# Kernel optimization log

Measured on AMD Instinct MI355X. Metric: run time of the kernel, lower is better.

## Reference

```python
import jax, jax.numpy as jnp
import numpy as np

B, OBS, ACT_DIM, C, CTX, H = 128, 512, 7, 100, 128, 512
IN = OBS + 1 + CTX  # states + scalar action component + context = 641


def cont2disc(values, n):
    return jnp.clip(jnp.floor((values + 1.0) / 2.0 * n), 0, n - 1)


def setup_inputs() -> dict:
    key = jax.random.key(0)
    ks = jax.random.split(key, 10)
    def w(k, shape):
        return jax.random.normal(k, shape, dtype=jnp.float32) / np.sqrt(shape[-2])
    return {
        "observations": jax.random.normal(ks[0], (B, OBS), dtype=jnp.float32),
        "actions": jax.random.uniform(ks[1], (B, ACT_DIM), dtype=jnp.float32, minval=-1.0, maxval=1.0),
        # one MLP per action dim (weight_sharing=False): layers IN->H->H->CTX
        "W1": w(ks[2], (ACT_DIM, IN, H)),  "b1": jnp.zeros((ACT_DIM, H), jnp.float32),
        "W2": w(ks[3], (ACT_DIM, H, H)),   "b2": jnp.zeros((ACT_DIM, H), jnp.float32),
        "W3": w(ks[4], (ACT_DIM, H, CTX)), "b3": jnp.zeros((ACT_DIM, CTX), jnp.float32),
        # output_proj = MLP((1,)): single dense CTX->1, no activation
        "Wp": w(ks[5], (CTX, 1)), "bp": jnp.zeros((1,), jnp.float32),
        "compute_lse": 1,
    }


def reference(observations, actions, W1, b1, W2, b2, W3, b3, Wp, bp, compute_lse):
    n = observations.shape[0]
    acts = cont2disc(actions, C)  # [B, ACT_DIM], float component indices
    context = jnp.zeros((n, CTX), observations.dtype)
    comp = jnp.arange(C, dtype=observations.dtype)  # candidate components 0..C-1
    q = jnp.zeros((n, ACT_DIM * C), observations.dtype)

    for i in range(1, ACT_DIM):
        def mlp(x, i=i):  # hidden layers relu, final layer linear
            h = jax.nn.relu(x @ W1[i] + b1[i])
            h = jax.nn.relu(h @ W2[i] + b2[i])
            return h @ W3[i] + b3[i]

        # batched over all num_components candidate actions (replaces the per-j loop)
        xin = jnp.concatenate([
            jnp.broadcast_to(observations[:, None, :], (n, C, OBS)),
            jnp.broadcast_to(comp[None, :, None], (n, C, 1)),
            jnp.broadcast_to(context[:, None, :], (n, C, CTX)),
        ], axis=-1)  # [B, C, IN]
        curr_ctx = mlp(xin) + context[:, None, :]        # [B, C, CTX]
        qv = (curr_ctx @ Wp + bp)[..., 0]                # [B, C]
        q = q.at[:, (i - 1) * C : i * C].set(qv)          # which_qval ordering

        # advance context with the actual (discretized) action
        x = jnp.concatenate([observations, acts[:, i:i + 1], context], axis=-1)
        context = mlp(x) + context

    if compute_lse:
        return jax.scipy.special.logsumexp(q, axis=-1)    # [B]
    return context @ Wp + bp                              # [B, 1]
```

## Files before the change

kernel.cpp:

```cpp
#include <hip/hip_runtime.h>
#include <math.h>

#define BATCH 128
#define ACT 7
#define NC 100
#define CTXD 128
#define HID 512
#define QW 600

typedef __attribute__((ext_vector_type(8))) __bf16 bf16x8;
typedef __attribute__((ext_vector_type(4))) float f32x4;
typedef __attribute__((ext_vector_type(4))) unsigned short u16x4;

__device__ __forceinline__ unsigned short f2bf(float f) {
    union { float f; unsigned int u; } v; v.f = f;
    unsigned int u = v.u;
    return (unsigned short)((u + 0x7fffu + ((u >> 16) & 1u)) >> 16);
}
__device__ __forceinline__ unsigned int pack2bf(float a, float b) {
    unsigned int ua = __float_as_uint(a) + 0x8000u;
    unsigned int ub = __float_as_uint(b) + 0x8000u;
    return (ua >> 16) | (ub & 0xffff0000u);
}

__device__ __forceinline__ void async16(const void* g, void* l) {
    __builtin_amdgcn_global_load_lds(
        (const __attribute__((address_space(1))) unsigned int*)(uintptr_t)g,
        (__attribute__((address_space(3))) unsigned int*)(unsigned int)(uintptr_t)l,
        16, 0, 0);
}

__global__ void prep_kernel(const float* __restrict__ obs, const float* __restrict__ W1,
                            const float* __restrict__ W2, const float* __restrict__ W3,
                            const float* __restrict__ Wp,
                            unsigned short* __restrict__ obs_bf, unsigned short* __restrict__ W1Cbf,
                            unsigned short* __restrict__ W2bf, unsigned short* __restrict__ W3bf,
                            unsigned short* __restrict__ W1AT, unsigned short* __restrict__ W2T,
                            float* __restrict__ vq) {
    const int bidx = blockIdx.x, tid = threadIdx.x;
    if (bidx < 2368) {
        const int e = (bidx * 256 + tid) * 4;
        const float* src; unsigned short* dst;
        if (e < 65536)        { src = obs + e; dst = obs_bf + e; }
        else if (e < 458752)  { int f = e - 65536; int i = f >> 16; int rem = f & 65535;
                                src = W1 + (size_t)(i + 1) * 328192 + 513*512 + rem; dst = W1Cbf + f; }
        else if (e < 2031616) { int f = e - 458752; src = W2 + 262144 + f; dst = W2bf + f; }
        else                  { int f = e - 2031616; src = W3 + 65536 + f; dst = W3bf + f; }
        float4 v = *(const float4*)src;
        u16x4 o; o[0] = f2bf(v.x); o[1] = f2bf(v.y); o[2] = f2bf(v.z); o[3] = f2bf(v.w);
        *(u16x4*)dst = o;
    } else if (bidx < 5440) {
        __shared__ float tile[32][33];
        const int idx = bidx - 2368;
        const int z = idx >> 8, rem = idx & 255;
        const int rb = rem & 15, cb = rem >> 4;
        const float* ip; unsigned short* op;
        if (z < 6) { ip = W1 + (size_t)(z + 1) * 328192; op = W1AT + (size_t)z * 262144; }
        else       { int i = z - 6; ip = W2 + (size_t)(i + 1) * 262144; op = W2T + (size_t)i * 262144; }
        const int r0 = rb * 32, c0 = cb * 32;
        const int tx = tid & 31, ty = tid >> 5;
        #pragma unroll
        for (int j = 0; j < 32; j += 8)
            tile[ty + j][tx] = ip[(size_t)(r0 + ty + j) * 512 + c0 + tx];
        __syncthreads();
        #pragma unroll
        for (int j = 0; j < 32; j += 8)
            op[(size_t)(c0 + ty + j) * 512 + r0 + tx] = f2bf(tile[tx][ty + j]);
    } else {
        const int idx = bidx - 5440;
        const int z = idx >> 1, k = (idx & 1) * 256 + tid;
        const float4* row = (const float4*)(W3 + (size_t)(z + 1) * 65536 + (size_t)k * 128);
        const float4* wp4 = (const float4*)Wp;
        float s = 0.f;
        #pragma unroll 8
        for (int n = 0; n < 32; ++n) {
            float4 a = row[n], w = wp4[n];
            s += a.x*w.x + a.y*w.y + a.z*w.z + a.w*w.w;
        }
        vq[z * 512 + k] = s;
    }
}

__launch_bounds__(256)
__global__ void yobs_kernel(const unsigned short* __restrict__ A,
                            const unsigned short* __restrict__ BtAll,
                            const float* __restrict__ b1,
                            float* __restrict__ Yobs) {
    __shared__ unsigned short As[64*32];
    __shared__ unsigned short Bs[128*32];
    const int m0 = blockIdx.x * 64;
    const int n0 = blockIdx.y * 128;
    const int z  = blockIdx.z;
    const unsigned short* Bt = BtAll + (size_t)z * 262144;
    const int tid = threadIdx.x, lane = tid & 63, wave = tid >> 6;
    const int wm = wave >> 1, wn = wave & 1;
    const int srow = tid >> 2, skc = (tid & 3) * 8;
    const unsigned short* gA  = A  + (size_t)(m0 + srow) * HID + skc;
    const unsigned short* gB0 = Bt + (size_t)(n0 + srow) * HID + skc;
    const unsigned short* gB1 = gB0 + 64 * HID;
    f32x4 acc[2][4] = {};
    for (int k0 = 0; k0 < HID; k0 += 32) {
        async16(gA + k0, As + tid*8);
        async16(gB0 + k0, Bs + tid*8);
        async16(gB1 + k0, Bs + 2048 + tid*8);
        __syncthreads();
        const int q8 = (lane >> 4) * 8, l15 = lane & 15;
        bf16x8 af[2], bfr[4];
        #pragma unroll
        for (int mt = 0; mt < 2; ++mt)
            af[mt] = *(const bf16x8*)(As + (wm*32 + mt*16 + l15) * 32 + q8);
        #pragma unroll
        for (int nt = 0; nt < 4; ++nt)
            bfr[nt] = *(const bf16x8*)(Bs + (wn*64 + nt*16 + l15) * 32 + q8);
        #pragma unroll
        for (int mt = 0; mt < 2; ++mt)
            #pragma unroll
            for (int nt = 0; nt < 4; ++nt)
                acc[mt][nt] = __builtin_amdgcn_mfma_f32_16x16x32_bf16(af[mt], bfr[nt], acc[mt][nt], 0, 0, 0);
        __syncthreads();
    }
    const int colL = wn*64 + (lane & 15);
    #pragma unroll
    for (int nt = 0; nt < 4; ++nt) {
        const int col = n0 + colL + nt*16;
        const float bb = b1[(z + 1) * HID + col];
        #pragma unroll
        for (int mt = 0; mt < 2; ++mt)
            #pragma unroll
            for (int r = 0; r < 4; ++r) {
                const int row = m0 + wm*32 + mt*16 + (lane >> 4)*4 + r;
                Yobs[(size_t)z * 65536 + (size_t)row * HID + col] = acc[mt][nt][r] + bb;
            }
    }
}

__launch_bounds__(1024)
__global__ void chain_kernel(const float* __restrict__ Yobs, const float* __restrict__ W1,
                             const unsigned short* __restrict__ W1Cbf,
                             const unsigned short* __restrict__ W2bf,
                             const unsigned short* __restrict__ W3bf,
                             const float* __restrict__ b2, const float* __restrict__ b3,
                             const float* __restrict__ actions,
                             const float* __restrict__ Wp, const float* __restrict__ bp,
                             float* __restrict__ Y0all, float* __restrict__ QOFF) {
    const int b = blockIdx.x, t = threadIdx.x;
    __shared__ float ctx[128], h1[512], h2s[512];
    __shared__ float part[2048];
    const int pair = t & 255, kq = t >> 8;
    const int pair3 = t & 63, kq3 = t >> 6;
    if (t < 128) ctx[t] = 0.f;
    __syncthreads();
    for (int i = 1; i <= 6; ++i) {
        if (t < 128) part[t] = (ctx[t] + b3[i*128 + t]) * Wp[t];
        __syncthreads();
        if (t < 64) {
            float v = part[t] + part[t + 64];
            #pragma unroll
            for (int o = 32; o > 0; o >>= 1) v += __shfl_down(v, o, 64);
            if (t == 0) QOFF[(i-1)*128 + b] = v + bp[0];
        }
        __syncthreads();
        const float a = actions[b*ACT + i];
        float fj = floorf((a + 1.0f) * 50.0f);
        fj = fminf(fmaxf(fj, 0.0f), 99.0f);
        {
            const unsigned int* wp1 = (const unsigned int*)(W1Cbf + (size_t)(i-1)*65536) + pair;
            float acc0 = 0.f, acc1 = 0.f;
            #pragma unroll 8
            for (int k = kq*32; k < kq*32 + 32; ++k) {
                unsigned int u = wp1[k*256];
                float c = ctx[k];
                acc0 = fmaf(c, __uint_as_float(u << 16), acc0);
                acc1 = fmaf(c, __uint_as_float(u & 0xffff0000u), acc1);
            }
            *(float2*)(&part[kq*512 + 2*pair]) = make_float2(acc0, acc1);
        }
        __syncthreads();
        if (t < 256) {
            const int n2 = 2*t;
            float2 p0 = *(const float2*)(&part[n2]);
            float2 p1 = *(const float2*)(&part[512 + n2]);
            float2 p2 = *(const float2*)(&part[1024 + n2]);
            float2 p3 = *(const float2*)(&part[1536 + n2]);
            float2 yo = *(const float2*)(Yobs + (size_t)(i-1)*65536 + b*512 + n2);
            float y0a = yo.x + p0.x + p1.x + p2.x + p3.x;
            float y0b = yo.y + p0.y + p1.y + p2.y + p3.y;
            *(float2*)(Y0all + (size_t)(i-1)*65536 + b*512 + n2) = make_float2(y0a, y0b);
            const float* w1a = W1 + (size_t)i*328192 + 262144;
            float2 wv = *(const float2*)(w1a + n2);
            h1[n2]   = fmaxf(fmaf(fj, wv.x, y0a), 0.f);
            h1[n2+1] = fmaxf(fmaf(fj, wv.y, y0b), 0.f);
        }
        __syncthreads();
        {
            const unsigned int* wp2 = (const unsigned int*)(W2bf + (size_t)(i-1)*262144) + pair;
            float acc0 = 0.f, acc1 = 0.f;
            #pragma unroll 16
            for (int k = kq*128; k < kq*128 + 128; ++k) {
                unsigned int u = wp2[k*256];
                float hv = h1[k];
                acc0 = fmaf(hv, __uint_as_float(u << 16), acc0);
                acc1 = fmaf(hv, __uint_as_float(u & 0xffff0000u), acc1);
            }
            *(float2*)(&part[kq*512 + 2*pair]) = make_float2(acc0, acc1);
        }
        __syncthreads();
        if (t < 256) {
            const int n2 = 2*t;
            float2 p0 = *(const float2*)(&part[n2]);
            float2 p1 = *(const float2*)(&part[512 + n2]);
            float2 p2 = *(const float2*)(&part[1024 + n2]);
            float2 p3 = *(const float2*)(&part[1536 + n2]);
            float2 bb = *(const float2*)(b2 + i*512 + n2);
            h2s[n2]   = fmaxf(p0.x + p1.x + p2.x + p3.x + bb.x, 0.f);
            h2s[n2+1] = fmaxf(p0.y + p1.y + p2.y + p3.y + bb.y, 0.f);
        }
        __syncthreads();
        {
            const unsigned int* wp3 = (const unsigned int*)(W3bf + (size_t)(i-1)*65536) + pair3;
            float acc0 = 0.f, acc1 = 0.f;
            #pragma unroll 8
            for (int k = kq3*32; k < kq3*32 + 32; ++k) {
                unsigned int u = wp3[k*64];
                float hv = h2s[k];
                acc0 = fmaf(hv, __uint_as_float(u << 16), acc0);
                acc1 = fmaf(hv, __uint_as_float(u & 0xffff0000u), acc1);
            }
            *(float2*)(&part[kq3*128 + 2*pair3]) = make_float2(acc0, acc1);
        }
        __syncthreads();
        if (t < 128) {
            float s = 0.f;
            #pragma unroll
            for (int qg = 0; qg < 16; ++qg) s += part[qg*128 + t];
            ctx[t] = s + b3[i*128 + t] + ctx[t];
        }
        __syncthreads();
    }
}

__global__ void h1all_kernel(const float* __restrict__ Y0all, const float* __restrict__ W1,
                             unsigned short* __restrict__ H1) {
    const int t = blockIdx.x * 256 + threadIdx.x;
    const int row = t >> 6, kc = (t & 63) << 3;
    const int z = row / 12800, rr = row - z * 12800;
    const int b = rr / 100;
    const float c = (float)(rr - b * 100);
    const float* yp = Y0all + (size_t)z*65536 + (size_t)b*512 + kc;
    const float* wp = W1 + (size_t)(z+1)*328192 + 262144 + kc;
    float4 ya = *(const float4*)(yp), yb = *(const float4*)(yp + 4);
    float4 wa = *(const float4*)(wp), wb = *(const float4*)(wp + 4);
    uint4 o;
    o.x = pack2bf(fmaxf(fmaf(c, wa.x, ya.x), 0.f), fmaxf(fmaf(c, wa.y, ya.y), 0.f));
    o.y = pack2bf(fmaxf(fmaf(c, wa.z, ya.z), 0.f), fmaxf(fmaf(c, wa.w, ya.w), 0.f));
    o.z = pack2bf(fmaxf(fmaf(c, wb.x, yb.x), 0.f), fmaxf(fmaf(c, wb.y, yb.y), 0.f));
    o.w = pack2bf(fmaxf(fmaf(c, wb.z, yb.z), 0.f), fmaxf(fmaf(c, wb.w, yb.w), 0.f));
    *(uint4*)(H1 + (size_t)row * 512 + kc) = o;
}

__launch_bounds__(512)
__global__ void gemm2q_kernel(const unsigned short* __restrict__ H1,
                              const unsigned short* __restrict__ W2T,
                              const float* __restrict__ b2,
                              const float* __restrict__ vq, float* __restrict__ qpart) {
    __shared__ __align__(16) unsigned short Ab[3][16384];
    __shared__ __align__(16) unsigned short Bb[3][8192];
    const int orig = blockIdx.x;
    const int wg = (orig & 7) * 150 + (orig >> 3);
    const int bn = wg & 3, mtile = wg >> 2;
    const int z  = mtile / 50;
    const int r0 = mtile * 256;
    const int n0 = bn * 128;
    const int tid = threadIdx.x, lane = tid & 63, wave = tid >> 6;
    const int wm = wave >> 1, wn = wave & 1;
    const int l15 = lane & 15, gq = lane >> 4;
    const int cb0 = (gq ^ (l15 & 7)) * 8;
    const int rw = tid >> 3;
    const int cbx = ((tid & 7) ^ (rw & 7)) * 8;
    const unsigned short* gA = H1 + (size_t)(r0 + rw) * 512 + cbx;
    const unsigned short* gB = W2T + (size_t)z * 262144 + (size_t)(n0 + rw) * 512 + cbx;
    f32x4 acc[4][4] = {};

#define STAGE2Q(kt, cbuf) do {                                               \
    const int k0_ = (kt) * 64;                                               \
    _Pragma("unroll")                                                        \
    for (int s = 0; s < 4; ++s)                                              \
        async16(gA + k0_ + s * 32768, &Ab[cbuf][(s * 512 + tid) * 8]);       \
    _Pragma("unroll")                                                        \
    for (int s = 0; s < 2; ++s)                                              \
        async16(gB + k0_ + s * 32768, &Bb[cbuf][(s * 512 + tid) * 8]);       \
} while (0)

    STAGE2Q(0, 0);
    STAGE2Q(1, 1);
    asm volatile("s_waitcnt vmcnt(6)" ::: "memory");
    __builtin_amdgcn_sched_barrier(0);
    __builtin_amdgcn_s_barrier();

    const int arow = (wm * 64 + l15) * 64;
    const int brow = (wn * 64 + l15) * 64;

    #pragma unroll
    for (int t = 0; t < 8; ++t) {
        const int c = t % 3;
        bf16x8 af[4], bfr[4];
        #pragma unroll
        for (int mt = 0; mt < 4; ++mt)
            af[mt] = *(const bf16x8*)(&Ab[c][arow + mt * 1024 + cb0]);
        #pragma unroll
        for (int nt = 0; nt < 4; ++nt)
            bfr[nt] = *(const bf16x8*)(&Bb[c][brow + nt * 1024 + cb0]);
        if (t < 6) STAGE2Q(t + 2, (t + 2) % 3);
        __builtin_amdgcn_s_setprio(1);
        #pragma unroll
        for (int mt = 0; mt < 4; ++mt)
            #pragma unroll
            for (int nt = 0; nt < 4; ++nt)
                acc[mt][nt] = __builtin_amdgcn_mfma_f32_16x16x32_bf16(af[mt], bfr[nt], acc[mt][nt], 0, 0, 0);
        __builtin_amdgcn_s_setprio(0);
        #pragma unroll
        for (int mt = 0; mt < 4; ++mt)
            af[mt] = *(const bf16x8*)(&Ab[c][arow + mt * 1024 + (cb0 ^ 32)]);
        #pragma unroll
        for (int nt = 0; nt < 4; ++nt)
            bfr[nt] = *(const bf16x8*)(&Bb[c][brow + nt * 1024 + (cb0 ^ 32)]);
        __builtin_amdgcn_s_setprio(1);
        #pragma unroll
        for (int mt = 0; mt < 4; ++mt)
            #pragma unroll
            for (int nt = 0; nt < 4; ++nt)
                acc[mt][nt] = __builtin_amdgcn_mfma_f32_16x16x32_bf16(af[mt], bfr[nt], acc[mt][nt], 0, 0, 0);
        __builtin_amdgcn_s_setprio(0);
        if (t < 7) {
            asm volatile("s_waitcnt lgkmcnt(0)" ::: "memory");
            if (t < 6)      asm volatile("s_waitcnt vmcnt(6)" ::: "memory");
            else            asm volatile("s_waitcnt vmcnt(0)" ::: "memory");
            __builtin_amdgcn_sched_barrier(0);
            __builtin_amdgcn_s_barrier();
        }
    }
#undef STAGE2Q

    float vb[4], bbv[4];
    #pragma unroll
    for (int nt = 0; nt < 4; ++nt) {
        const int col = n0 + wn * 64 + nt * 16 + l15;
        bbv[nt] = b2[(z + 1) * 512 + col];
        vb[nt]  = vq[z * 512 + col];
    }
    const int plane2 = bn * 2 + wn;
    #pragma unroll
    for (int mt = 0; mt < 4; ++mt)
        #pragma unroll
        for (int r = 0; r < 4; ++r) {
            float p = 0.f;
            #pragma unroll
            for (int nt = 0; nt < 4; ++nt)
                p = fmaf(fmaxf(acc[mt][nt][r] + bbv[nt], 0.f), vb[nt], p);
            p += __shfl_xor(p, 1, 64);
            p += __shfl_xor(p, 2, 64);
            p += __shfl_xor(p, 4, 64);
            p += __shfl_xor(p, 8, 64);
            if (l15 == 0) {
                const int grow = r0 + wm * 64 + mt * 16 + gq * 4 + r;
                qpart[(size_t)plane2 * 76800 + grow] = p;
            }
        }
}

__global__ void lse_kernel(const float* __restrict__ qpart, const float* __restrict__ QOFF,
                           float* __restrict__ out) {
    __shared__ float red[256];
    __shared__ float qs[QW];
    const int b = blockIdx.x, t = threadIdx.x;
    for (int k = t; k < QW; k += 256) {
        const int z = k / 100, gc = k - z * 100;
        const int grow = z * 12800 + b * 100 + gc;
        float s = QOFF[z * 128 + b];
        #pragma unroll
        for (int p = 0; p < 8; ++p) s += qpart[(size_t)p * 76800 + grow];
        qs[k] = s;
    }
    __syncthreads();
    float m = 0.0f;
    for (int k = t; k < QW; k += 256) m = fmaxf(m, qs[k]);
    red[t] = m; __syncthreads();
    for (int s = 128; s > 0; s >>= 1) { if (t < s) red[t] = fmaxf(red[t], red[t+s]); __syncthreads(); }
    m = red[0]; __syncthreads();
    float sum = 0.0f;
    for (int k = t; k < QW; k += 256) sum += expf(qs[k] - m);
    red[t] = sum; __syncthreads();
    for (int s = 128; s > 0; s >>= 1) { if (t < s) red[t] += red[t+s]; __syncthreads(); }
    if (t == 0) out[b] = logf(red[0] + 100.0f * expf(-m)) + m;
}

extern "C" void kernel_launch(void* const* d_in, const int* in_sizes, int n_in,
                              void* d_out, int out_size, void* d_ws, size_t ws_size,
                              hipStream_t stream) {
    const float* obs     = (const float*)d_in[0];
    const float* actions = (const float*)d_in[1];
    const float* W1      = (const float*)d_in[2];
    const float* b1      = (const float*)d_in[3];
    const float* W2      = (const float*)d_in[4];
    const float* b2      = (const float*)d_in[5];
    const float* W3      = (const float*)d_in[6];
    const float* b3      = (const float*)d_in[7];
    const float* Wp      = (const float*)d_in[8];
    const float* bp      = (const float*)d_in[9];
    float* out = (float*)d_out;
    float* ws  = (float*)d_ws;

    unsigned short* obs_bf = (unsigned short*)(ws);
    unsigned short* W1AT   = (unsigned short*)(ws + 32768);
    unsigned short* W2T    = (unsigned short*)(ws + 819200);
    unsigned short* W1Cbf  = (unsigned short*)(ws + 1605632);
    unsigned short* W2bf   = (unsigned short*)(ws + 1802240);
    unsigned short* W3bf   = (unsigned short*)(ws + 2588672);
    float* Yobs  = ws + 2785280;
    float* Y0all = ws + 3178496;
    float* QOFF  = ws + 3571712;
    float* vq    = ws + 3572736;
    float* qpart = ws + 3575808;
    unsigned short* H1 = (unsigned short*)(ws + 4190208);

    prep_kernel<<<5452, 256, 0, stream>>>(obs, W1, W2, W3, Wp,
                                          obs_bf, W1Cbf, W2bf, W3bf, W1AT, W2T, vq);
    yobs_kernel<<<dim3(2,4,6), 256, 0, stream>>>(obs_bf, W1AT, b1, Yobs);
    chain_kernel<<<BATCH, 1024, 0, stream>>>(Yobs, W1, W1Cbf, W2bf, W3bf, b2, b3, actions, Wp, bp, Y0all, QOFF);
    h1all_kernel<<<19200, 256, 0, stream>>>(Y0all, W1, H1);
    gemm2q_kernel<<<1200, 512, 0, stream>>>(H1, W2T, b2, vq, qpart);
    lse_kernel<<<BATCH, 256, 0, stream>>>(qpart, QOFF, out);
}
```

Baseline: 225.4 us.

## Restructure gemm2q main loop into quadrant-phased ping-pong schedule with double buffering

Changes the shared-memory pipeline of the second GEMM from triple to double buffering and splits each K-step into four MFMA quadrant phases separated by workgroup barriers. LDS fragment reads for later quadrants are interleaved with MFMAs of earlier quadrants, and global prefetch of the next tile is issued into the just-freed buffer mid-iteration. The intent is to cut LDS footprint for higher occupancy and overlap LDS reads with matrix-core work. In exchange it adds many more barriers per iteration and a shorter prefetch distance.

```diff
diff --git a/kernel.cpp b/kernel.cpp
--- a/kernel.cpp
+++ b/kernel.cpp
@@ -263,8 +263,8 @@
                               const unsigned short* __restrict__ W2T,
                               const float* __restrict__ b2,
                               const float* __restrict__ vq, float* __restrict__ qpart) {
-    __shared__ __align__(16) unsigned short Ab[3][16384];
-    __shared__ __align__(16) unsigned short Bb[3][8192];
+    __shared__ __align__(16) unsigned short Ab[2][16384];
+    __shared__ __align__(16) unsigned short Bb[2][8192];
     const int orig = blockIdx.x;
     const int wg = (orig & 7) * 150 + (orig >> 3);
     const int bn = wg & 3, mtile = wg >> 2;
@@ -280,6 +280,7 @@
     const unsigned short* gA = H1 + (size_t)(r0 + rw) * 512 + cbx;
     const unsigned short* gB = W2T + (size_t)z * 262144 + (size_t)(n0 + rw) * 512 + cbx;
     f32x4 acc[4][4] = {};
+    bf16x8 af[4][2], bfr[4][2];
 
 #define STAGE2Q(kt, cbuf) do {                                               \
     const int k0_ = (kt) * 64;                                               \
@@ -291,55 +292,73 @@
         async16(gB + k0_ + s * 32768, &Bb[cbuf][(s * 512 + tid) * 8]);       \
 } while (0)
 
+    const int arow = (wm * 64 + l15) * 64;
+    const int brow = (wn * 64 + l15) * 64;
+
+#define RD_A(mt) do {                                                        \
+    af[mt][0] = *(const bf16x8*)(&Ab[c][arow + (mt) * 1024 + cb0]);          \
+    af[mt][1] = *(const bf16x8*)(&Ab[c][arow + (mt) * 1024 + (cb0 ^ 32)]);   \
+} while (0)
+#define RD_B(nt) do {                                                        \
+    bfr[nt][0] = *(const bf16x8*)(&Bb[c][brow + (nt) * 1024 + cb0]);         \
+    bfr[nt][1] = *(const bf16x8*)(&Bb[c][brow + (nt) * 1024 + (cb0 ^ 32)]);  \
+} while (0)
+#define MM(mt, nt) do {                                                      \
+    acc[mt][nt] = __builtin_amdgcn_mfma_f32_16x16x32_bf16(af[mt][0], bfr[nt][0], acc[mt][nt], 0, 0, 0); \
+    acc[mt][nt] = __builtin_amdgcn_mfma_f32_16x16x32_bf16(af[mt][1], bfr[nt][1], acc[mt][nt], 0, 0, 0); \
+} while (0)
+#define LEAD_BAR() do {                                                      \
+    __builtin_amdgcn_s_barrier();                                            \
+    asm volatile("s_waitcnt lgkmcnt(0)" ::: "memory");                       \
+    __builtin_amdgcn_sched_barrier(0);                                       \
+} while (0)
+
     STAGE2Q(0, 0);
     STAGE2Q(1, 1);
     asm volatile("s_waitcnt vmcnt(6)" ::: "memory");
     __builtin_amdgcn_sched_barrier(0);
     __builtin_amdgcn_s_barrier();
 
-    const int arow = (wm * 64 + l15) * 64;
-    const int brow = (wn * 64 + l15) * 64;
-
     #pragma unroll
     for (int t = 0; t < 8; ++t) {
-        const int c = t % 3;
-        bf16x8 af[4], bfr[4];
-        #pragma unroll
-        for (int mt = 0; mt < 4; ++mt)
-            af[mt] = *(const bf16x8*)(&Ab[c][arow + mt * 1024 + cb0]);
-        #pragma unroll
-        for (int nt = 0; nt < 4; ++nt)
-            bfr[nt] = *(const bf16x8*)(&Bb[c][brow + nt * 1024 + cb0]);
-        if (t < 6) STAGE2Q(t + 2, (t + 2) % 3);
+        const int c = t & 1;
+        RD_A(0); RD_A(1); RD_B(0); RD_B(1);
+        LEAD_BAR();
         __builtin_amdgcn_s_setprio(1);
-        #pragma unroll
-        for (int mt = 0; mt < 4; ++mt)
-            #pragma unroll
-            for (int nt = 0; nt < 4; ++nt)
-                acc[mt][nt] = __builtin_amdgcn_mfma_f32_16x16x32_bf16(af[mt], bfr[nt], acc[mt][nt], 0, 0, 0);
+        MM(0,0); MM(0,1); MM(1,0); MM(1,1);
         __builtin_amdgcn_s_setprio(0);
-        #pragma unroll
-        for (int mt = 0; mt < 4; ++mt)
-            af[mt] = *(const bf16x8*)(&Ab[c][arow + mt * 1024 + (cb0 ^ 32)]);
-        #pragma unroll
-        for (int nt = 0; nt < 4; ++nt)
-            bfr[nt] = *(const bf16x8*)(&Bb[c][brow + nt * 1024 + (cb0 ^ 32)]);
+        __builtin_amdgcn_s_barrier();
+        RD_B(2); RD_B(3);
+        LEAD_BAR();
         __builtin_amdgcn_s_setprio(1);
-        #pragma unroll
-        for (int mt = 0; mt < 4; ++mt)
-            #pragma unroll
-            for (int nt = 0; nt < 4; ++nt)
-                acc[mt][nt] = __builtin_amdgcn_mfma_f32_16x16x32_bf16(af[mt], bfr[nt], acc[mt][nt], 0, 0, 0);
+        MM(0,2); MM(0,3); MM(1,2); MM(1,3);
         __builtin_amdgcn_s_setprio(0);
-        if (t < 7) {
-            asm volatile("s_waitcnt lgkmcnt(0)" ::: "memory");
-            if (t < 6)      asm volatile("s_waitcnt vmcnt(6)" ::: "memory");
-            else            asm volatile("s_waitcnt vmcnt(0)" ::: "memory");
+        __builtin_amdgcn_s_barrier();
+        RD_A(2); RD_A(3);
+        LEAD_BAR();
+        __builtin_amdgcn_s_setprio(1);
+        MM(2,0); MM(2,1); MM(3,0); MM(3,1);
+        __builtin_amdgcn_s_setprio(0);
+        __builtin_amdgcn_s_barrier();
+        if (t < 6) {
+            STAGE2Q(t + 2, c);
+            asm volatile("s_waitcnt vmcnt(6)" ::: "memory");
             __builtin_amdgcn_sched_barrier(0);
-            __builtin_amdgcn_s_barrier();
-        }
+        } else if (t == 6) {
+            asm volatile("s_waitcnt vmcnt(0)" ::: "memory");
+            __builtin_amdgcn_sched_barrier(0);
+        }
+        __builtin_amdgcn_s_barrier();
+        __builtin_amdgcn_s_setprio(1);
+        MM(2,2); MM(2,3); MM(3,2); MM(3,3);
+        __builtin_amdgcn_s_setprio(0);
+        __builtin_amdgcn_s_barrier();
     }
 #undef STAGE2Q
+#undef RD_A
+#undef RD_B
+#undef MM
+#undef LEAD_BAR
 
     float vb[4], bbv[4];
     #pragma unroll
```

Result: slower. 233.7 us (+3.7%).

## Fuse H1 generation into the layer-2 GEMM and keep the full W2 tile in LDS

Applied to the files above, without the earlier changes.

Removes the separate h1all kernel that materialised the bf16 H1 activations in global memory. The GEMM now builds its A fragments in registers from Y0all, the component index and a W1 row (fma, relu, bf16 pack). The whole 128x512 W2T slice is preloaded into LDS once instead of being triple-buffered per K step. This saves a large global write and read of H1 and one launch, but adds ALU work and global loads inside the MFMA loop, drops the async pipelining, and uses 128KB of LDS per block, which limits occupancy.

```diff
diff --git a/kernel.cpp b/kernel.cpp
--- a/kernel.cpp
+++ b/kernel.cpp
@@ -239,107 +239,91 @@
     }
 }
 
-__global__ void h1all_kernel(const float* __restrict__ Y0all, const float* __restrict__ W1,
-                             unsigned short* __restrict__ H1) {
-    const int t = blockIdx.x * 256 + threadIdx.x;
-    const int row = t >> 6, kc = (t & 63) << 3;
-    const int z = row / 12800, rr = row - z * 12800;
-    const int b = rr / 100;
-    const float c = (float)(rr - b * 100);
-    const float* yp = Y0all + (size_t)z*65536 + (size_t)b*512 + kc;
-    const float* wp = W1 + (size_t)(z+1)*328192 + 262144 + kc;
-    float4 ya = *(const float4*)(yp), yb = *(const float4*)(yp + 4);
-    float4 wa = *(const float4*)(wp), wb = *(const float4*)(wp + 4);
-    uint4 o;
-    o.x = pack2bf(fmaxf(fmaf(c, wa.x, ya.x), 0.f), fmaxf(fmaf(c, wa.y, ya.y), 0.f));
-    o.y = pack2bf(fmaxf(fmaf(c, wa.z, ya.z), 0.f), fmaxf(fmaf(c, wa.w, ya.w), 0.f));
-    o.z = pack2bf(fmaxf(fmaf(c, wb.x, yb.x), 0.f), fmaxf(fmaf(c, wb.y, yb.y), 0.f));
-    o.w = pack2bf(fmaxf(fmaf(c, wb.z, yb.z), 0.f), fmaxf(fmaf(c, wb.w, yb.w), 0.f));
-    *(uint4*)(H1 + (size_t)row * 512 + kc) = o;
-}
-
 __launch_bounds__(512)
-__global__ void gemm2q_kernel(const unsigned short* __restrict__ H1,
+__global__ void gemm2q_kernel(const float* __restrict__ Y0all,
+                              const float* __restrict__ W1,
                               const unsigned short* __restrict__ W2T,
                               const float* __restrict__ b2,
                               const float* __restrict__ vq, float* __restrict__ qpart) {
-    __shared__ __align__(16) unsigned short Ab[3][16384];
-    __shared__ __align__(16) unsigned short Bb[3][8192];
+    __shared__ __align__(16) unsigned short Bs[65536];
     const int orig = blockIdx.x;
     const int wg = (orig & 7) * 150 + (orig >> 3);
     const int bn = wg & 3, mtile = wg >> 2;
     const int z  = mtile / 50;
     const int r0 = mtile * 256;
+    const int zrow0 = (mtile - z * 50) * 256;
     const int n0 = bn * 128;
     const int tid = threadIdx.x, lane = tid & 63, wave = tid >> 6;
     const int wm = wave >> 1, wn = wave & 1;
     const int l15 = lane & 15, gq = lane >> 4;
-    const int cb0 = (gq ^ (l15 & 7)) * 8;
-    const int rw = tid >> 3;
-    const int cbx = ((tid & 7) ^ (rw & 7)) * 8;
-    const unsigned short* gA = H1 + (size_t)(r0 + rw) * 512 + cbx;
-    const unsigned short* gB = W2T + (size_t)z * 262144 + (size_t)(n0 + rw) * 512 + cbx;
+
+    {
+        const unsigned short* gBrow = W2T + (size_t)z * 262144
+            + (size_t)(n0 + wave) * 512 + ((lane & ~7) | ((lane & 7) ^ wave)) * 8;
+        #pragma unroll
+        for (int s = 0; s < 16; ++s)
+            async16(gBrow + s * 8 * 512, Bs + ((size_t)(s * 512 + tid)) * 8);
+        asm volatile("s_waitcnt vmcnt(0)" ::: "memory");
+        __syncthreads();
+    }
+
+    const float* yb_[4]; float cf[4];
+    #pragma unroll
+    for (int mt = 0; mt < 4; ++mt) {
+        const int lrow = wm * 64 + mt * 16 + l15;
+        const int zr = zrow0 + lrow;
+        const int b = zr / 100;
+        cf[mt] = (float)(zr - 100 * b);
+        yb_[mt] = Y0all + (size_t)z * 65536 + (size_t)b * 512 + gq * 8;
+    }
+    const float* wb_ = W1 + (size_t)(z + 1) * 328192 + 262144 + gq * 8;
+
+    int boff[4][2];
+    #pragma unroll
+    for (int nt = 0; nt < 4; ++nt) {
+        const int nn = wn * 64 + nt * 16 + l15;
+        #pragma unroll
+        for (int h = 0; h < 2; ++h)
+            boff[nt][h] = nn * 512 + (((h * 4 + gq) ^ (l15 & 7))) * 8;
+    }
+
     f32x4 acc[4][4] = {};
-
-#define STAGE2Q(kt, cbuf) do {                                               \
-    const int k0_ = (kt) * 64;                                               \
-    _Pragma("unroll")                                                        \
-    for (int s = 0; s < 4; ++s)                                              \
-        async16(gA + k0_ + s * 32768, &Ab[cbuf][(s * 512 + tid) * 8]);       \
-    _Pragma("unroll")                                                        \
-    for (int s = 0; s < 2; ++s)                                              \
-        async16(gB + k0_ + s * 32768, &Bb[cbuf][(s * 512 + tid) * 8]);       \
-} while (0)
-
-    STAGE2Q(0, 0);
-    STAGE2Q(1, 1);
-    asm volatile("s_waitcnt vmcnt(6)" ::: "memory");
-    __builtin_amdgcn_sched_barrier(0);
-    __builtin_amdgcn_s_barrier();
-
-    const int arow = (wm * 64 + l15) * 64;
-    const int brow = (wn * 64 + l15) * 64;
-
     #pragma unroll
     for (int t = 0; t < 8; ++t) {
-        const int c = t % 3;
-        bf16x8 af[4], bfr[4];
+        bf16x8 af[4][2], bfr[4][2];
+        #pragma unroll
+        for (int nt = 0; nt < 4; ++nt) {
+            bfr[nt][0] = *(const bf16x8*)(Bs + boff[nt][0] + t * 64);
+            bfr[nt][1] = *(const bf16x8*)(Bs + boff[nt][1] + t * 64);
+        }
+        #pragma unroll
+        for (int h = 0; h < 2; ++h) {
+            const float* w = wb_ + t * 64 + h * 32;
+            const float4 wa = *(const float4*)w, wv = *(const float4*)(w + 4);
+            #pragma unroll
+            for (int mt = 0; mt < 4; ++mt) {
+                const float* y = yb_[mt] + t * 64 + h * 32;
+                const float4 ya = *(const float4*)y, yv = *(const float4*)(y + 4);
+                const float c = cf[mt];
+                uint4 o;
+                o.x = pack2bf(fmaxf(fmaf(c, wa.x, ya.x), 0.f), fmaxf(fmaf(c, wa.y, ya.y), 0.f));
+                o.y = pack2bf(fmaxf(fmaf(c, wa.z, ya.z), 0.f), fmaxf(fmaf(c, wa.w, ya.w), 0.f));
+                o.z = pack2bf(fmaxf(fmaf(c, wv.x, yv.x), 0.f), fmaxf(fmaf(c, wv.y, yv.y), 0.f));
+                o.w = pack2bf(fmaxf(fmaf(c, wv.z, yv.z), 0.f), fmaxf(fmaf(c, wv.w, yv.w), 0.f));
+                union { uint4 u; bf16x8 v; } cvt; cvt.u = o;
+                af[mt][h] = cvt.v;
+            }
+        }
+        __builtin_amdgcn_s_setprio(1);
         #pragma unroll
         for (int mt = 0; mt < 4; ++mt)
-            af[mt] = *(const bf16x8*)(&Ab[c][arow + mt * 1024 + cb0]);
-        #pragma unroll
-        for (int nt = 0; nt < 4; ++nt)
-            bfr[nt] = *(const bf16x8*)(&Bb[c][brow + nt * 1024 + cb0]);
-        if (t < 6) STAGE2Q(t + 2, (t + 2) % 3);
-        __builtin_amdgcn_s_setprio(1);
-        #pragma unroll
-        for (int mt = 0; mt < 4; ++mt)
-            #pragma unroll
-            for (int nt = 0; nt < 4; ++nt)
-                acc[mt][nt] = __builtin_amdgcn_mfma_f32_16x16x32_bf16(af[mt], bfr[nt], acc[mt][nt], 0, 0, 0);
+            #pragma unroll
+            for (int nt = 0; nt < 4; ++nt) {
+                acc[mt][nt] = __builtin_amdgcn_mfma_f32_16x16x32_bf16(af[mt][0], bfr[nt][0], acc[mt][nt], 0, 0, 0);
+                acc[mt][nt] = __builtin_amdgcn_mfma_f32_16x16x32_bf16(af[mt][1], bfr[nt][1], acc[mt][nt], 0, 0, 0);
+            }
         __builtin_amdgcn_s_setprio(0);
-        #pragma unroll
-        for (int mt = 0; mt < 4; ++mt)
-            af[mt] = *(const bf16x8*)(&Ab[c][arow + mt * 1024 + (cb0 ^ 32)]);
-        #pragma unroll
-        for (int nt = 0; nt < 4; ++nt)
-            bfr[nt] = *(const bf16x8*)(&Bb[c][brow + nt * 1024 + (cb0 ^ 32)]);
-        __builtin_amdgcn_s_setprio(1);
-        #pragma unroll
-        for (int mt = 0; mt < 4; ++mt)
-            #pragma unroll
-            for (int nt = 0; nt < 4; ++nt)
-                acc[mt][nt] = __builtin_amdgcn_mfma_f32_16x16x32_bf16(af[mt], bfr[nt], acc[mt][nt], 0, 0, 0);
-        __builtin_amdgcn_s_setprio(0);
-        if (t < 7) {
-            asm volatile("s_waitcnt lgkmcnt(0)" ::: "memory");
-            if (t < 6)      asm volatile("s_waitcnt vmcnt(6)" ::: "memory");
-            else            asm volatile("s_waitcnt vmcnt(0)" ::: "memory");
-            __builtin_amdgcn_sched_barrier(0);
-            __builtin_amdgcn_s_barrier();
-        }
-    }
-#undef STAGE2Q
+    }
 
     float vb[4], bbv[4];
     #pragma unroll
@@ -421,13 +405,11 @@
     float* QOFF  = ws + 3571712;
     float* vq    = ws + 3572736;
     float* qpart = ws + 3575808;
-    unsigned short* H1 = (unsigned short*)(ws + 4190208);
 
     prep_kernel<<<5452, 256, 0, stream>>>(obs, W1, W2, W3, Wp,
                                           obs_bf, W1Cbf, W2bf, W3bf, W1AT, W2T, vq);
     yobs_kernel<<<dim3(2,4,6), 256, 0, stream>>>(obs_bf, W1AT, b1, Yobs);
     chain_kernel<<<BATCH, 1024, 0, stream>>>(Yobs, W1, W1Cbf, W2bf, W3bf, b2, b3, actions, Wp, bp, Y0all, QOFF);
-    h1all_kernel<<<19200, 256, 0, stream>>>(Y0all, W1, H1);
-    gemm2q_kernel<<<1200, 512, 0, stream>>>(H1, W2T, b2, vq, qpart);
+    gemm2q_kernel<<<1200, 512, 0, stream>>>(Y0all, W1, W2T, b2, vq, qpart);
     lse_kernel<<<BATCH, 256, 0, stream>>>(qpart, QOFF, out);
 }
```

New measurement: 245.4 us. 1.09x slower.

## Preload full B tile into LDS and stream A fragments directly from global

Applied to the files above, without the earlier changes.

The GEMM2 kernel now loads the entire 128x512 W2T slice for its column block into LDS once, with a single wait and barrier. It drops the triple-buffered A/B LDS pipeline and its per-iteration barriers. A fragments are read straight from global memory into registers, with the next k-step register-prefetched (afc/afn). This removes the per-stage barriers and LDS staging of A, but uses 128KB of LDS, which may cut occupancy. Uncoalesced direct global A loads may also expose memory latency.

```diff
diff --git a/kernel.cpp b/kernel.cpp
--- a/kernel.cpp
+++ b/kernel.cpp
@@ -263,8 +263,7 @@
                               const unsigned short* __restrict__ W2T,
                               const float* __restrict__ b2,
                               const float* __restrict__ vq, float* __restrict__ qpart) {
-    __shared__ __align__(16) unsigned short Ab[3][16384];
-    __shared__ __align__(16) unsigned short Bb[3][8192];
+    __shared__ __align__(16) unsigned short Bs[65536];
     const int orig = blockIdx.x;
     const int wg = (orig & 7) * 150 + (orig >> 3);
     const int bn = wg & 3, mtile = wg >> 2;
@@ -274,72 +273,67 @@
     const int tid = threadIdx.x, lane = tid & 63, wave = tid >> 6;
     const int wm = wave >> 1, wn = wave & 1;
     const int l15 = lane & 15, gq = lane >> 4;
-    const int cb0 = (gq ^ (l15 & 7)) * 8;
-    const int rw = tid >> 3;
-    const int cbx = ((tid & 7) ^ (rw & 7)) * 8;
-    const unsigned short* gA = H1 + (size_t)(r0 + rw) * 512 + cbx;
-    const unsigned short* gB = W2T + (size_t)z * 262144 + (size_t)(n0 + rw) * 512 + cbx;
+
+    {
+        const unsigned short* gbase = W2T + (size_t)z * 262144
+            + (size_t)(n0 + (tid >> 3)) * 512 + ((lane & 7) ^ (lane >> 3)) * 8;
+        #pragma unroll
+        for (int j = 0; j < 16; ++j) {
+            const int t = j >> 1, half = j & 1;
+            async16(gbase + half * 32768 + t * 64,
+                    Bs + t * 8192 + half * 4096 + tid * 8);
+        }
+        asm volatile("s_waitcnt vmcnt(0)" ::: "memory");
+        __syncthreads();
+    }
+
+    int boff[4][2];
+    #pragma unroll
+    for (int nt = 0; nt < 4; ++nt) {
+        const int nn = wn * 64 + nt * 16 + l15;
+        #pragma unroll
+        for (int h = 0; h < 2; ++h)
+            boff[nt][h] = nn * 64 + (((h * 4 + gq) ^ (l15 & 7))) * 8;
+    }
+    const unsigned short* aptr = H1 + (size_t)(r0 + wm * 64 + l15) * 512 + gq * 8;
+
     f32x4 acc[4][4] = {};
-
-#define STAGE2Q(kt, cbuf) do {                                               \
-    const int k0_ = (kt) * 64;                                               \
-    _Pragma("unroll")                                                        \
-    for (int s = 0; s < 4; ++s)                                              \
-        async16(gA + k0_ + s * 32768, &Ab[cbuf][(s * 512 + tid) * 8]);       \
-    _Pragma("unroll")                                                        \
-    for (int s = 0; s < 2; ++s)                                              \
-        async16(gB + k0_ + s * 32768, &Bb[cbuf][(s * 512 + tid) * 8]);       \
-} while (0)
-
-    STAGE2Q(0, 0);
-    STAGE2Q(1, 1);
-    asm volatile("s_waitcnt vmcnt(6)" ::: "memory");
-    __builtin_amdgcn_sched_barrier(0);
-    __builtin_amdgcn_s_barrier();
-
-    const int arow = (wm * 64 + l15) * 64;
-    const int brow = (wn * 64 + l15) * 64;
+    bf16x8 afc[4][2], afn[4][2], bfr[4][2];
+    #pragma unroll
+    for (int mt = 0; mt < 4; ++mt)
+        #pragma unroll
+        for (int h = 0; h < 2; ++h)
+            afc[mt][h] = *(const bf16x8*)(aptr + mt * 8192 + h * 32);
 
     #pragma unroll
     for (int t = 0; t < 8; ++t) {
-        const int c = t % 3;
-        bf16x8 af[4], bfr[4];
+        #pragma unroll
+        for (int nt = 0; nt < 4; ++nt)
+            #pragma unroll
+            for (int h = 0; h < 2; ++h)
+                bfr[nt][h] = *(const bf16x8*)(Bs + t * 8192 + boff[nt][h]);
+        if (t < 7) {
+            #pragma unroll
+            for (int mt = 0; mt < 4; ++mt)
+                #pragma unroll
+                for (int h = 0; h < 2; ++h)
+                    afn[mt][h] = *(const bf16x8*)(aptr + mt * 8192 + (t + 1) * 64 + h * 32);
+        }
+        __builtin_amdgcn_s_setprio(1);
         #pragma unroll
         for (int mt = 0; mt < 4; ++mt)
-            af[mt] = *(const bf16x8*)(&Ab[c][arow + mt * 1024 + cb0]);
-        #pragma unroll
-        for (int nt = 0; nt < 4; ++nt)
-            bfr[nt] = *(const bf16x8*)(&Bb[c][brow + nt * 1024 + cb0]);
-        if (t < 6) STAGE2Q(t + 2, (t + 2) % 3);
-        __builtin_amdgcn_s_setprio(1);
+            #pragma unroll
+            for (int nt = 0; nt < 4; ++nt) {
+                acc[mt][nt] = __builtin_amdgcn_mfma_f32_16x16x32_bf16(afc[mt][0], bfr[nt][0], acc[mt][nt], 0, 0, 0);
+                acc[mt][nt] = __builtin_amdgcn_mfma_f32_16x16x32_bf16(afc[mt][1], bfr[nt][1], acc[mt][nt], 0, 0, 0);
+            }
+        __builtin_amdgcn_s_setprio(0);
         #pragma unroll
         for (int mt = 0; mt < 4; ++mt)
             #pragma unroll
-            for (int nt = 0; nt < 4; ++nt)
-                acc[mt][nt] = __builtin_amdgcn_mfma_f32_16x16x32_bf16(af[mt], bfr[nt], acc[mt][nt], 0, 0, 0);
-        __builtin_amdgcn_s_setprio(0);
-        #pragma unroll
-        for (int mt = 0; mt < 4; ++mt)
-            af[mt] = *(const bf16x8*)(&Ab[c][arow + mt * 1024 + (cb0 ^ 32)]);
-        #pragma unroll
-        for (int nt = 0; nt < 4; ++nt)
-            bfr[nt] = *(const bf16x8*)(&Bb[c][brow + nt * 1024 + (cb0 ^ 32)]);
-        __builtin_amdgcn_s_setprio(1);
-        #pragma unroll
-        for (int mt = 0; mt < 4; ++mt)
-            #pragma unroll
-            for (int nt = 0; nt < 4; ++nt)
-                acc[mt][nt] = __builtin_amdgcn_mfma_f32_16x16x32_bf16(af[mt], bfr[nt], acc[mt][nt], 0, 0, 0);
-        __builtin_amdgcn_s_setprio(0);
-        if (t < 7) {
-            asm volatile("s_waitcnt lgkmcnt(0)" ::: "memory");
-            if (t < 6)      asm volatile("s_waitcnt vmcnt(6)" ::: "memory");
-            else            asm volatile("s_waitcnt vmcnt(0)" ::: "memory");
-            __builtin_amdgcn_sched_barrier(0);
-            __builtin_amdgcn_s_barrier();
-        }
-    }
-#undef STAGE2Q
+            for (int h = 0; h < 2; ++h)
+                afc[mt][h] = afn[mt][h];
+    }
 
     float vb[4], bbv[4];
     #pragma unroll
```

After: 269.7 us. 19.7% more time.
